# Kernel tuning notes

Hardware: AMD Instinct MI355X
Metric: run time of the kernel (lower is better)

Reference implementation:

```python
import jax, jax.numpy as jnp
import numpy as np
from jax import lax

IN_CH, OUT_CH, K = 64, 64, 3
FAN_IN = 8           # LogicNets-style fan-in per output channel (over C_in*K taps)
IN_SCALE, IN_BITS = 0.0625, 8
OUT_SCALE, OUT_BITS = 0.125, 8


def make_mask(seed=7):
    # Binary mask [OUT_CH, IN_CH, K] with exactly FAN_IN ones per output channel
    rng = np.random.RandomState(seed)
    m = np.zeros((OUT_CH, IN_CH * K), dtype=np.float32)
    for o in range(OUT_CH):
        idx = rng.choice(IN_CH * K, size=FAN_IN, replace=False)
        m[o, idx] = 1.0
    return jnp.asarray(m.reshape(OUT_CH, IN_CH, K))


def fake_quant(v, scale, bits):
    # symmetric fake quantization with straight-through estimator
    qmin = -(2 ** (bits - 1))
    qmax = 2 ** (bits - 1) - 1
    q = jnp.clip(jnp.round(v / scale), qmin, qmax) * scale
    return v + lax.stop_gradient(q - v)


def setup_inputs() -> dict:
    key = jax.random.key(0)
    k1, k2 = jax.random.split(key)
    x = jax.random.normal(k1, (512, IN_CH, 1024), dtype=jnp.float32)
    weight = jax.random.normal(k2, (OUT_CH, IN_CH, K), dtype=jnp.float32) * 0.1
    mask = make_mask()
    return {"x": x, "weight": weight, "mask": mask}


def reference(x, weight, mask):
    # input quant
    xq = fake_quant(x, IN_SCALE, IN_BITS)
    # masked (sparse) conv1d, padding=1 (same length)
    w = weight * mask
    out = lax.conv_general_dilated(
        xq, w,
        window_strides=(1,),
        padding=[(1, 1)],
        dimension_numbers=("NCH", "OIH", "NCH"),
    )
    # output quant
    return fake_quant(out, OUT_SCALE, OUT_BITS)
```

## Files before the change

### kernel.cpp

```cpp
#include <hip/hip_runtime.h>

namespace {
constexpr int kInCh  = 64;
constexpr int kOutCh = 64;
constexpr int kK     = 3;
constexpr int kFanIn = 8;
constexpr int kH     = 1024;
constexpr int kTile  = 128;
constexpr int kRow   = kTile + 8;
constexpr int kBlk   = 512;
}

struct Tap { int off; float w; };

__device__ __forceinline__ float quant_in(float v) {
    float q = rintf(v * 16.0f);
    q = fmaxf(q, -128.0f);
    q = fminf(q, 127.0f);
    return q * 0.0625f;
}

__device__ __forceinline__ float quant_out(float v) {
    float q = rintf(v * 8.0f);
    q = fmaxf(q, -128.0f);
    q = fminf(q, 127.0f);
    return q * 0.125f;
}

__global__ void prep_taps(const float* __restrict__ weight,
                          const float* __restrict__ mask,
                          Tap* __restrict__ taps) {
    __shared__ unsigned long long bal[3];
    const int o    = blockIdx.x;
    const int j    = threadIdx.x;
    const int k    = j >> 6;
    const int ci   = j & 63;
    const int idx  = (o * kInCh + ci) * kK + k;

    const float m = mask[idx];
    const unsigned long long b = __ballot(m != 0.0f);
    if (ci == 0) bal[k] = b;
    __syncthreads();

    const unsigned long long lower = b & ((1ull << ci) - 1ull);
    int rank = __popcll(lower);
    #pragma unroll
    for (int w = 0; w < kK; ++w) if (w < k) rank += __popcll(bal[w]);

    if (m != 0.0f && rank < kFanIn) {
        taps[o * kFanIn + rank].off = (ci * kRow + k + 3) * 4;
        taps[o * kFanIn + rank].w   = weight[idx] * m;
    }
    int total = __popcll(bal[0]) + __popcll(bal[1]) + __popcll(bal[2]);
    if (j >= total && j < kFanIn) {
        taps[o * kFanIn + j].off = 3 * 4;
        taps[o * kFanIn + j].w   = 0.0f;
    }
}

__global__ __launch_bounds__(kBlk, 8) void sparse_conv(
        const float* __restrict__ x,
        const Tap*   __restrict__ taps,
        float*       __restrict__ out) {
    __shared__ float sm[kInCh * kRow];

    const int t    = threadIdx.x;
    const int lane = t & 63;
    const int g    = __builtin_amdgcn_readfirstlane(t >> 6);
    const int h0   = blockIdx.x * kTile;
    const int n    = blockIdx.y;
    const float* __restrict__ xn = x + (size_t)n * kInCh * kH;

    const Tap  myTap = taps[g * 64 + lane];
    const int   vOff = myTap.off;
    const int   vW   = __float_as_int(myTap.w);

    #pragma unroll
    for (int it = 0; it < 4; ++it) {
        int f  = it * kBlk + t;
        int ci = f >> 5;
        int c4 = f & 31;
        float4 v = reinterpret_cast<const float4*>(xn + ci * kH + h0)[c4];
        v.x = quant_in(v.x); v.y = quant_in(v.y);
        v.z = quant_in(v.z); v.w = quant_in(v.w);
        reinterpret_cast<float4*>(&sm[ci * kRow + 4])[c4] = v;
    }
    if (t < 64) {
        int ci = t;
        float4 v = make_float4(0.f, 0.f, 0.f, 0.f);
        if (h0 > 0) v = *reinterpret_cast<const float4*>(xn + ci * kH + h0 - 4);
        v.x = quant_in(v.x); v.y = quant_in(v.y);
        v.z = quant_in(v.z); v.w = quant_in(v.w);
        *reinterpret_cast<float4*>(&sm[ci * kRow]) = v;
    } else if (t < 128) {
        int ci = t - 64;
        float4 v = make_float4(0.f, 0.f, 0.f, 0.f);
        if (h0 + kTile < kH) v = *reinterpret_cast<const float4*>(xn + ci * kH + h0 + kTile);
        v.x = quant_in(v.x); v.y = quant_in(v.y);
        v.z = quant_in(v.z); v.w = quant_in(v.w);
        *reinterpret_cast<float4*>(&sm[ci * kRow + 4 + kTile]) = v;
    }
    __syncthreads();

    const int i  = t & 63;
    const int i4 = i << 2;
    float* __restrict__ outn = out + (size_t)n * kOutCh * kH + h0;
    const char* smb = reinterpret_cast<const char*>(sm);

    #pragma unroll 2
    for (int oo = 0; oo < 8; ++oo) {
        int o = g * 8 + oo;

        float acc0 = 0.f, acc1 = 0.f;
        #pragma unroll
        for (int j = 0; j < kFanIn; ++j) {
            const int l   = oo * 8 + j;
            const int off = __builtin_amdgcn_readlane(vOff, l);
            const float w = __int_as_float(__builtin_amdgcn_readlane(vW, l));
            const float a0 = *reinterpret_cast<const float*>(smb + off + i4);
            const float a1 = *reinterpret_cast<const float*>(smb + off + i4 + 256);
            acc0 = fmaf(w, a0, acc0);
            acc1 = fmaf(w, a1, acc1);
        }
        outn[o * kH + i]      = quant_out(acc0);
        outn[o * kH + i + 64] = quant_out(acc1);
    }
}

extern "C" void kernel_launch(void* const* d_in, const int* in_sizes, int n_in,
                              void* d_out, int out_size, void* d_ws, size_t ws_size,
                              hipStream_t stream) {
    const float* x      = (const float*)d_in[0];
    const float* weight = (const float*)d_in[1];
    const float* mask   = (const float*)d_in[2];
    float* out = (float*)d_out;
    Tap* taps = (Tap*)d_ws;

    const int nBatch = in_sizes[0] / (kInCh * kH);

    prep_taps<<<kOutCh, kInCh * kK, 0, stream>>>(weight, mask, taps);
    dim3 grid(kH / kTile, nBatch);
    sparse_conv<<<grid, kBlk, 0, stream>>>(x, taps, out);
}
```

Baseline: 238.2 us.

## Fuse tap prep into persistent conv kernel with register-prefetched next tile

Removes the separate prep_taps launch by having each block build the sparse tap table in shared memory with ballots. The conv kernel becomes persistent (up to 1024 blocks striding over tiles) and prefetches the next tile's input into registers while computing the current one. The input-quant scale is folded into the weights. This adds per-block table construction and register pressure under the 8-blocks launch bound, and relies on the mask having at most 8 nonzeros per row, with no zero padding of unused tap slots.

Result: slower. 249.7 us (+4.8%).

```diff
diff --git a/kernel.cpp b/kernel.cpp
--- a/kernel.cpp
+++ b/kernel.cpp
@@ -9,15 +9,16 @@
 constexpr int kTile  = 128;
 constexpr int kRow   = kTile + 8;
 constexpr int kBlk   = 512;
+constexpr int kHB    = kH / kTile;
+constexpr int kGrid  = 1024;
 }
 
 struct Tap { int off; float w; };
 
-__device__ __forceinline__ float quant_in(float v) {
+__device__ __forceinline__ float quant_in_i(float v) {
     float q = rintf(v * 16.0f);
     q = fmaxf(q, -128.0f);
-    q = fminf(q, 127.0f);
-    return q * 0.0625f;
+    return fminf(q, 127.0f);
 }
 
 __device__ __forceinline__ float quant_out(float v) {
@@ -27,104 +28,137 @@
     return q * 0.125f;
 }
 
-__global__ void prep_taps(const float* __restrict__ weight,
-                          const float* __restrict__ mask,
-                          Tap* __restrict__ taps) {
-    __shared__ unsigned long long bal[3];
-    const int o    = blockIdx.x;
-    const int j    = threadIdx.x;
-    const int k    = j >> 6;
-    const int ci   = j & 63;
-    const int idx  = (o * kInCh + ci) * kK + k;
-
-    const float m = mask[idx];
-    const unsigned long long b = __ballot(m != 0.0f);
-    if (ci == 0) bal[k] = b;
-    __syncthreads();
-
-    const unsigned long long lower = b & ((1ull << ci) - 1ull);
-    int rank = __popcll(lower);
-    #pragma unroll
-    for (int w = 0; w < kK; ++w) if (w < k) rank += __popcll(bal[w]);
-
-    if (m != 0.0f && rank < kFanIn) {
-        taps[o * kFanIn + rank].off = (ci * kRow + k + 3) * 4;
-        taps[o * kFanIn + rank].w   = weight[idx] * m;
-    }
-    int total = __popcll(bal[0]) + __popcll(bal[1]) + __popcll(bal[2]);
-    if (j >= total && j < kFanIn) {
-        taps[o * kFanIn + j].off = 3 * 4;
-        taps[o * kFanIn + j].w   = 0.0f;
-    }
-}
-
 __global__ __launch_bounds__(kBlk, 8) void sparse_conv(
         const float* __restrict__ x,
-        const Tap*   __restrict__ taps,
-        float*       __restrict__ out) {
+        const float* __restrict__ weight,
+        const float* __restrict__ mask,
+        float*       __restrict__ out,
+        int nTiles) {
     __shared__ float sm[kInCh * kRow];
+    __shared__ Tap   tbl[kBlk];
 
     const int t    = threadIdx.x;
     const int lane = t & 63;
-    const int g    = __builtin_amdgcn_readfirstlane(t >> 6);
-    const int h0   = blockIdx.x * kTile;
-    const int n    = blockIdx.y;
-    const float* __restrict__ xn = x + (size_t)n * kInCh * kH;
+    const int g    = t >> 6;
 
-    const Tap  myTap = taps[g * 64 + lane];
-    const int   vOff = myTap.off;
-    const int   vW   = __float_as_int(myTap.w);
-
-    #pragma unroll
-    for (int it = 0; it < 4; ++it) {
-        int f  = it * kBlk + t;
-        int ci = f >> 5;
-        int c4 = f & 31;
-        float4 v = reinterpret_cast<const float4*>(xn + ci * kH + h0)[c4];
-        v.x = quant_in(v.x); v.y = quant_in(v.y);
-        v.z = quant_in(v.z); v.w = quant_in(v.w);
-        reinterpret_cast<float4*>(&sm[ci * kRow + 4])[c4] = v;
-    }
-    if (t < 64) {
-        int ci = t;
-        float4 v = make_float4(0.f, 0.f, 0.f, 0.f);
-        if (h0 > 0) v = *reinterpret_cast<const float4*>(xn + ci * kH + h0 - 4);
-        v.x = quant_in(v.x); v.y = quant_in(v.y);
-        v.z = quant_in(v.z); v.w = quant_in(v.w);
-        *reinterpret_cast<float4*>(&sm[ci * kRow]) = v;
-    } else if (t < 128) {
-        int ci = t - 64;
-        float4 v = make_float4(0.f, 0.f, 0.f, 0.f);
-        if (h0 + kTile < kH) v = *reinterpret_cast<const float4*>(xn + ci * kH + h0 + kTile);
-        v.x = quant_in(v.x); v.y = quant_in(v.y);
-        v.z = quant_in(v.z); v.w = quant_in(v.w);
-        *reinterpret_cast<float4*>(&sm[ci * kRow + 4 + kTile]) = v;
+    {
+        const unsigned long long low = (1ull << lane) - 1ull;
+        #pragma unroll
+        for (int oo = 0; oo < 8; ++oo) {
+            const int o    = g * 8 + oo;
+            const int base = (o * kInCh + lane) * kK;
+            const float m0 = mask[base + 0], m1 = mask[base + 1], m2 = mask[base + 2];
+            const float w0 = weight[base + 0], w1 = weight[base + 1], w2 = weight[base + 2];
+            const unsigned long long b0 = __ballot(m0 != 0.0f);
+            const unsigned long long b1 = __ballot(m1 != 0.0f);
+            const unsigned long long b2 = __ballot(m2 != 0.0f);
+            const int n0 = __popcll(b0), n1 = __popcll(b1);
+            if (m0 != 0.0f) { int r = __popcll(b0 & low);
+                tbl[o * kFanIn + r].off = (lane * kRow + 3) * 4;
+                tbl[o * kFanIn + r].w   = w0 * m0 * 0.0625f; }
+            if (m1 != 0.0f) { int r = n0 + __popcll(b1 & low);
+                tbl[o * kFanIn + r].off = (lane * kRow + 4) * 4;
+                tbl[o * kFanIn + r].w   = w1 * m1 * 0.0625f; }
+            if (m2 != 0.0f) { int r = n0 + n1 + __popcll(b2 & low);
+                tbl[o * kFanIn + r].off = (lane * kRow + 5) * 4;
+                tbl[o * kFanIn + r].w   = w2 * m2 * 0.0625f; }
+        }
     }
     __syncthreads();
+    const int vOff = tbl[t].off;
+    const int vW   = __float_as_int(tbl[t].w);
 
-    const int i  = t & 63;
-    const int i4 = i << 2;
-    float* __restrict__ outn = out + (size_t)n * kOutCh * kH + h0;
+    const int tci = t >> 5;
+    const int c4  = t & 31;
+    const int i4  = lane << 2;
+
+    float4 r0, r1, r2, r3, rh;
+    const float4 z4 = make_float4(0.f, 0.f, 0.f, 0.f);
+
+#define ISSUE_LOADS(TAU)                                                          \
+    {                                                                             \
+        const int   n_  = (TAU) >> 3;                                             \
+        const int   h0_ = ((TAU) & (kHB - 1)) * kTile;                            \
+        const float* p_ = x + ((size_t)n_ * kInCh) * kH + h0_;                    \
+        r0 = reinterpret_cast<const float4*>(p_ + (tci     ) * kH)[c4];           \
+        r1 = reinterpret_cast<const float4*>(p_ + (tci + 16) * kH)[c4];           \
+        r2 = reinterpret_cast<const float4*>(p_ + (tci + 32) * kH)[c4];           \
+        r3 = reinterpret_cast<const float4*>(p_ + (tci + 48) * kH)[c4];           \
+        if (t < 64) {                                                             \
+            rh = (h0_ > 0) ? *reinterpret_cast<const float4*>(p_ + t * kH - 4)    \
+                           : z4;                                                  \
+        } else if (t < 128) {                                                     \
+            rh = (h0_ + kTile < kH)                                               \
+                 ? *reinterpret_cast<const float4*>(p_ + (t - 64) * kH + kTile)   \
+                 : z4;                                                            \
+        }                                                                         \
+    }
+
+#define STAGE()                                                                   \
+    {                                                                             \
+        float4 q_;                                                                \
+        q_.x = quant_in_i(r0.x); q_.y = quant_in_i(r0.y);                         \
+        q_.z = quant_in_i(r0.z); q_.w = quant_in_i(r0.w);                         \
+        reinterpret_cast<float4*>(&sm[(tci     ) * kRow + 4])[c4] = q_;           \
+        q_.x = quant_in_i(r1.x); q_.y = quant_in_i(r1.y);                         \
+        q_.z = quant_in_i(r1.z); q_.w = quant_in_i(r1.w);                         \
+        reinterpret_cast<float4*>(&sm[(tci + 16) * kRow + 4])[c4] = q_;           \
+        q_.x = quant_in_i(r2.x); q_.y = quant_in_i(r2.y);                         \
+        q_.z = quant_in_i(r2.z); q_.w = quant_in_i(r2.w);                         \
+        reinterpret_cast<float4*>(&sm[(tci + 32) * kRow + 4])[c4] = q_;           \
+        q_.x = quant_in_i(r3.x); q_.y = quant_in_i(r3.y);                         \
+        q_.z = quant_in_i(r3.z); q_.w = quant_in_i(r3.w);                         \
+        reinterpret_cast<float4*>(&sm[(tci + 48) * kRow + 4])[c4] = q_;           \
+        if (t < 64) {                                                             \
+            float4 h_;                                                            \
+            h_.x = quant_in_i(rh.x); h_.y = quant_in_i(rh.y);                     \
+            h_.z = quant_in_i(rh.z); h_.w = quant_in_i(rh.w);                     \
+            *reinterpret_cast<float4*>(&sm[t * kRow]) = h_;                       \
+        } else if (t < 128) {                                                     \
+            float4 h_;                                                            \
+            h_.x = quant_in_i(rh.x); h_.y = quant_in_i(rh.y);                     \
+            h_.z = quant_in_i(rh.z); h_.w = quant_in_i(rh.w);                     \
+            *reinterpret_cast<float4*>(&sm[(t - 64) * kRow + 4 + kTile]) = h_;    \
+        }                                                                         \
+    }
+
+    int tau = blockIdx.x;
+    const int stride = gridDim.x;
     const char* smb = reinterpret_cast<const char*>(sm);
 
-    #pragma unroll 2
-    for (int oo = 0; oo < 8; ++oo) {
-        int o = g * 8 + oo;
+    ISSUE_LOADS(tau);
+    while (tau < nTiles) {
+        STAGE();
+        __syncthreads();
 
-        float acc0 = 0.f, acc1 = 0.f;
-        #pragma unroll
-        for (int j = 0; j < kFanIn; ++j) {
-            const int l   = oo * 8 + j;
-            const int off = __builtin_amdgcn_readlane(vOff, l);
-            const float w = __int_as_float(__builtin_amdgcn_readlane(vW, l));
-            const float a0 = *reinterpret_cast<const float*>(smb + off + i4);
-            const float a1 = *reinterpret_cast<const float*>(smb + off + i4 + 256);
-            acc0 = fmaf(w, a0, acc0);
-            acc1 = fmaf(w, a1, acc1);
+        const int nxt = tau + stride;
+        if (nxt < nTiles) ISSUE_LOADS(nxt);
+
+        float* __restrict__ outn =
+            out + ((size_t)(tau >> 3) * kOutCh) * kH + (tau & (kHB - 1)) * kTile;
+
+        #pragma unroll 2
+        for (int oo = 0; oo < 8; ++oo) {
+            const int o = g * 8 + oo;
+            float acc0 = 0.f, acc1 = 0.f;
+            #pragma unroll
+            for (int j = 0; j < kFanIn; ++j) {
+                const int l   = oo * 8 + j;
+                const int off = __builtin_amdgcn_readlane(vOff, l);
+                const float w = __int_as_float(__builtin_amdgcn_readlane(vW, l));
+                const float a0 = *reinterpret_cast<const float*>(smb + off + i4);
+                const float a1 = *reinterpret_cast<const float*>(smb + off + i4 + 256);
+                acc0 = fmaf(w, a0, acc0);
+                acc1 = fmaf(w, a1, acc1);
+            }
+            outn[o * kH + lane]      = quant_out(acc0);
+            outn[o * kH + lane + 64] = quant_out(acc1);
         }
-        outn[o * kH + i]      = quant_out(acc0);
-        outn[o * kH + i + 64] = quant_out(acc1);
+        __syncthreads();
+        tau = nxt;
     }
+#undef ISSUE_LOADS
+#undef STAGE
 }
 
 extern "C" void kernel_launch(void* const* d_in, const int* in_sizes, int n_in,
@@ -134,11 +168,10 @@
     const float* weight = (const float*)d_in[1];
     const float* mask   = (const float*)d_in[2];
     float* out = (float*)d_out;
-    Tap* taps = (Tap*)d_ws;
 
     const int nBatch = in_sizes[0] / (kInCh * kH);
+    const int nTiles = nBatch * kHB;
+    const int grid   = nTiles < kGrid ? nTiles : kGrid;
 
-    prep_taps<<<kOutCh, kInCh * kK, 0, stream>>>(weight, mask, taps);
-    dim3 grid(kH / kTile, nBatch);
-    sparse_conv<<<grid, kBlk, 0, stream>>>(x, taps, out);
+    sparse_conv<<<grid, kBlk, 0, stream>>>(x, weight, mask, out, nTiles);
 }
```

## Fuse tap preparation into conv kernel and double spatial tile size

Applied to the files above, without the earlier changes.

Removes the separate prep_taps launch: each block builds the sparse tap table in shared memory from weight and mask using wave ballots, and folds the input dequant scale into the weights. The tile grows to 256 positions, so each thread computes four outputs per channel, and all input loads are issued into registers before the table build to overlap latency. The grid is flattened to 1D. In exchange every block rereads the mask and weights, uses more registers and shared memory, and occupancy is lower with launch bounds reduced to 4.

Result: slower. 257.9 us (+8.3%).

```diff
diff --git a/kernel.cpp b/kernel.cpp
--- a/kernel.cpp
+++ b/kernel.cpp
@@ -6,18 +6,18 @@
 constexpr int kK     = 3;
 constexpr int kFanIn = 8;
 constexpr int kH     = 1024;
-constexpr int kTile  = 128;
+constexpr int kTile  = 256;
 constexpr int kRow   = kTile + 8;
 constexpr int kBlk   = 512;
+constexpr int kHB    = kH / kTile;
 }
 
 struct Tap { int off; float w; };
 
-__device__ __forceinline__ float quant_in(float v) {
+__device__ __forceinline__ float quant_in_i(float v) {
     float q = rintf(v * 16.0f);
     q = fmaxf(q, -128.0f);
-    q = fminf(q, 127.0f);
-    return q * 0.0625f;
+    return fminf(q, 127.0f);
 }
 
 __device__ __forceinline__ float quant_out(float v) {
@@ -27,103 +27,102 @@
     return q * 0.125f;
 }
 
-__global__ void prep_taps(const float* __restrict__ weight,
-                          const float* __restrict__ mask,
-                          Tap* __restrict__ taps) {
-    __shared__ unsigned long long bal[3];
-    const int o    = blockIdx.x;
-    const int j    = threadIdx.x;
-    const int k    = j >> 6;
-    const int ci   = j & 63;
-    const int idx  = (o * kInCh + ci) * kK + k;
-
-    const float m = mask[idx];
-    const unsigned long long b = __ballot(m != 0.0f);
-    if (ci == 0) bal[k] = b;
-    __syncthreads();
-
-    const unsigned long long lower = b & ((1ull << ci) - 1ull);
-    int rank = __popcll(lower);
-    #pragma unroll
-    for (int w = 0; w < kK; ++w) if (w < k) rank += __popcll(bal[w]);
-
-    if (m != 0.0f && rank < kFanIn) {
-        taps[o * kFanIn + rank].off = (ci * kRow + k + 3) * 4;
-        taps[o * kFanIn + rank].w   = weight[idx] * m;
-    }
-    int total = __popcll(bal[0]) + __popcll(bal[1]) + __popcll(bal[2]);
-    if (j >= total && j < kFanIn) {
-        taps[o * kFanIn + j].off = 3 * 4;
-        taps[o * kFanIn + j].w   = 0.0f;
-    }
-}
-
-__global__ __launch_bounds__(kBlk, 8) void sparse_conv(
+__global__ __launch_bounds__(kBlk, 4) void sparse_conv(
         const float* __restrict__ x,
-        const Tap*   __restrict__ taps,
+        const float* __restrict__ weight,
+        const float* __restrict__ mask,
         float*       __restrict__ out) {
     __shared__ float sm[kInCh * kRow];
+    __shared__ Tap   tbl[kBlk];
 
     const int t    = threadIdx.x;
     const int lane = t & 63;
     const int g    = __builtin_amdgcn_readfirstlane(t >> 6);
-    const int h0   = blockIdx.x * kTile;
-    const int n    = blockIdx.y;
-    const float* __restrict__ xn = x + (size_t)n * kInCh * kH;
+    const int tau  = blockIdx.x;
+    const int n    = tau >> 2;
+    const int h0   = (tau & (kHB - 1)) * kTile;
+    const float* __restrict__ xn = x + (size_t)n * kInCh * kH + h0;
 
-    const Tap  myTap = taps[g * 64 + lane];
-    const int   vOff = myTap.off;
-    const int   vW   = __float_as_int(myTap.w);
+    float4 r[8];
+    #pragma unroll
+    for (int it = 0; it < 8; ++it)
+        r[it] = reinterpret_cast<const float4*>(xn + (it * 8 + g) * kH)[lane];
+    float4 rh = make_float4(0.f, 0.f, 0.f, 0.f);
+    if (t < 64) {
+        if (h0 > 0) rh = *reinterpret_cast<const float4*>(xn + t * kH - 4);
+    } else if (t < 128) {
+        if (h0 + kTile < kH) rh = *reinterpret_cast<const float4*>(xn + (t - 64) * kH + kTile);
+    }
+
+    {
+        const unsigned long long low = (1ull << lane) - 1ull;
+        #pragma unroll
+        for (int oo = 0; oo < 8; ++oo) {
+            const int o    = g * 8 + oo;
+            const int base = (o * kInCh + lane) * kK;
+            const float m0 = mask[base + 0], m1 = mask[base + 1], m2 = mask[base + 2];
+            const float w0 = weight[base + 0], w1 = weight[base + 1], w2 = weight[base + 2];
+            const unsigned long long b0 = __ballot(m0 != 0.0f);
+            const unsigned long long b1 = __ballot(m1 != 0.0f);
+            const unsigned long long b2 = __ballot(m2 != 0.0f);
+            const int n0 = __popcll(b0), n1 = __popcll(b1);
+            if (m0 != 0.0f) { int rk = __popcll(b0 & low);
+                tbl[o * kFanIn + rk].off = (lane * kRow + 3) * 4;
+                tbl[o * kFanIn + rk].w   = w0 * m0 * 0.0625f; }
+            if (m1 != 0.0f) { int rk = n0 + __popcll(b1 & low);
+                tbl[o * kFanIn + rk].off = (lane * kRow + 4) * 4;
+                tbl[o * kFanIn + rk].w   = w1 * m1 * 0.0625f; }
+            if (m2 != 0.0f) { int rk = n0 + n1 + __popcll(b2 & low);
+                tbl[o * kFanIn + rk].off = (lane * kRow + 5) * 4;
+                tbl[o * kFanIn + rk].w   = w2 * m2 * 0.0625f; }
+        }
+    }
+    const int vOff = tbl[t].off;
+    const int vW   = __float_as_int(tbl[t].w);
 
     #pragma unroll
-    for (int it = 0; it < 4; ++it) {
-        int f  = it * kBlk + t;
-        int ci = f >> 5;
-        int c4 = f & 31;
-        float4 v = reinterpret_cast<const float4*>(xn + ci * kH + h0)[c4];
-        v.x = quant_in(v.x); v.y = quant_in(v.y);
-        v.z = quant_in(v.z); v.w = quant_in(v.w);
-        reinterpret_cast<float4*>(&sm[ci * kRow + 4])[c4] = v;
+    for (int it = 0; it < 8; ++it) {
+        float4 q;
+        q.x = quant_in_i(r[it].x); q.y = quant_in_i(r[it].y);
+        q.z = quant_in_i(r[it].z); q.w = quant_in_i(r[it].w);
+        reinterpret_cast<float4*>(&sm[(it * 8 + g) * kRow + 4])[lane] = q;
     }
     if (t < 64) {
-        int ci = t;
-        float4 v = make_float4(0.f, 0.f, 0.f, 0.f);
-        if (h0 > 0) v = *reinterpret_cast<const float4*>(xn + ci * kH + h0 - 4);
-        v.x = quant_in(v.x); v.y = quant_in(v.y);
-        v.z = quant_in(v.z); v.w = quant_in(v.w);
-        *reinterpret_cast<float4*>(&sm[ci * kRow]) = v;
+        float4 q;
+        q.x = quant_in_i(rh.x); q.y = quant_in_i(rh.y);
+        q.z = quant_in_i(rh.z); q.w = quant_in_i(rh.w);
+        *reinterpret_cast<float4*>(&sm[t * kRow]) = q;
     } else if (t < 128) {
-        int ci = t - 64;
-        float4 v = make_float4(0.f, 0.f, 0.f, 0.f);
-        if (h0 + kTile < kH) v = *reinterpret_cast<const float4*>(xn + ci * kH + h0 + kTile);
-        v.x = quant_in(v.x); v.y = quant_in(v.y);
-        v.z = quant_in(v.z); v.w = quant_in(v.w);
-        *reinterpret_cast<float4*>(&sm[ci * kRow + 4 + kTile]) = v;
+        float4 q;
+        q.x = quant_in_i(rh.x); q.y = quant_in_i(rh.y);
+        q.z = quant_in_i(rh.z); q.w = quant_in_i(rh.w);
+        *reinterpret_cast<float4*>(&sm[(t - 64) * kRow + 4 + kTile]) = q;
     }
     __syncthreads();
 
-    const int i  = t & 63;
-    const int i4 = i << 2;
+    const int i4 = lane << 2;
+    const char* smb = reinterpret_cast<const char*>(sm);
     float* __restrict__ outn = out + (size_t)n * kOutCh * kH + h0;
-    const char* smb = reinterpret_cast<const char*>(sm);
 
     #pragma unroll 2
     for (int oo = 0; oo < 8; ++oo) {
-        int o = g * 8 + oo;
-
-        float acc0 = 0.f, acc1 = 0.f;
+        const int o = g * 8 + oo;
+        float a0 = 0.f, a1 = 0.f, a2 = 0.f, a3 = 0.f;
         #pragma unroll
         for (int j = 0; j < kFanIn; ++j) {
             const int l   = oo * 8 + j;
             const int off = __builtin_amdgcn_readlane(vOff, l);
             const float w = __int_as_float(__builtin_amdgcn_readlane(vW, l));
-            const float a0 = *reinterpret_cast<const float*>(smb + off + i4);
-            const float a1 = *reinterpret_cast<const float*>(smb + off + i4 + 256);
-            acc0 = fmaf(w, a0, acc0);
-            acc1 = fmaf(w, a1, acc1);
+            const char* p = smb + off + i4;
+            a0 = fmaf(w, *reinterpret_cast<const float*>(p      ), a0);
+            a1 = fmaf(w, *reinterpret_cast<const float*>(p + 256), a1);
+            a2 = fmaf(w, *reinterpret_cast<const float*>(p + 512), a2);
+            a3 = fmaf(w, *reinterpret_cast<const float*>(p + 768), a3);
         }
-        outn[o * kH + i]      = quant_out(acc0);
-        outn[o * kH + i + 64] = quant_out(acc1);
+        outn[o * kH + lane]       = quant_out(a0);
+        outn[o * kH + lane +  64] = quant_out(a1);
+        outn[o * kH + lane + 128] = quant_out(a2);
+        outn[o * kH + lane + 192] = quant_out(a3);
     }
 }
 
@@ -134,11 +133,9 @@
     const float* weight = (const float*)d_in[1];
     const float* mask   = (const float*)d_in[2];
     float* out = (float*)d_out;
-    Tap* taps = (Tap*)d_ws;
 
     const int nBatch = in_sizes[0] / (kInCh * kH);
+    const int grid   = nBatch * kHB;
 
-    prep_taps<<<kOutCh, kInCh * kK, 0, stream>>>(weight, mask, taps);
-    dim3 grid(kH / kTile, nBatch);
-    sparse_conv<<<grid, kBlk, 0, stream>>>(x, taps, out);
+    sparse_conv<<<grid, kBlk, 0, stream>>>(x, weight, mask, out);
 }
```

## Halve tile and block size, batch global loads, fold input scale into weights

Applied to the files above, without the earlier changes.

Cuts the spatial tile to 64 and the block to 256 threads, so each wave handles 16 output channels with one accumulator per lane. All global loads are issued into registers before quantization and the LDS stores, so more loads are in flight. Halo loads shrink to single scalars. Taps are now read straight from global memory with uniform addresses instead of readlane broadcasts, and the input scale 1/16 is folded into the weights so the LDS holds integer-valued floats. This doubles the number of blocks and the halo overhead per tile, and tap loads now go through the scalar cache.

After: 238.1 us. Within noise of the previous version (-0.0%).

```diff
diff --git a/kernel.cpp b/kernel.cpp
--- a/kernel.cpp
+++ b/kernel.cpp
@@ -6,18 +6,18 @@
 constexpr int kK     = 3;
 constexpr int kFanIn = 8;
 constexpr int kH     = 1024;
-constexpr int kTile  = 128;
+constexpr int kTile  = 64;
 constexpr int kRow   = kTile + 8;
-constexpr int kBlk   = 512;
+constexpr int kBlk   = 256;
+constexpr int kHB    = kH / kTile;
 }
 
 struct Tap { int off; float w; };
 
-__device__ __forceinline__ float quant_in(float v) {
+__device__ __forceinline__ float quant_in_i(float v) {
     float q = rintf(v * 16.0f);
     q = fmaxf(q, -128.0f);
-    q = fminf(q, 127.0f);
-    return q * 0.0625f;
+    return fminf(q, 127.0f);
 }
 
 __device__ __forceinline__ float quant_out(float v) {
@@ -48,12 +48,12 @@
     for (int w = 0; w < kK; ++w) if (w < k) rank += __popcll(bal[w]);
 
     if (m != 0.0f && rank < kFanIn) {
-        taps[o * kFanIn + rank].off = (ci * kRow + k + 3) * 4;
-        taps[o * kFanIn + rank].w   = weight[idx] * m;
+        taps[o * kFanIn + rank].off = ci * kRow + k + 3;
+        taps[o * kFanIn + rank].w   = weight[idx] * m * 0.0625f;
     }
     int total = __popcll(bal[0]) + __popcll(bal[1]) + __popcll(bal[2]);
     if (j >= total && j < kFanIn) {
-        taps[o * kFanIn + j].off = 3 * 4;
+        taps[o * kFanIn + j].off = 3;
         taps[o * kFanIn + j].w   = 0.0f;
     }
 }
@@ -69,61 +69,52 @@
     const int g    = __builtin_amdgcn_readfirstlane(t >> 6);
     const int h0   = blockIdx.x * kTile;
     const int n    = blockIdx.y;
-    const float* __restrict__ xn = x + (size_t)n * kInCh * kH;
+    const float* __restrict__ xn = x + (size_t)n * kInCh * kH + h0;
 
-    const Tap  myTap = taps[g * 64 + lane];
-    const int   vOff = myTap.off;
-    const int   vW   = __float_as_int(myTap.w);
+    float4 r[4];
+    #pragma unroll
+    for (int it = 0; it < 4; ++it) {
+        const int f  = it * kBlk + t;
+        const int ci = f >> 4;
+        const int c4 = f & 15;
+        r[it] = reinterpret_cast<const float4*>(xn + ci * kH)[c4];
+    }
+    float hv = 0.f;
+    if (t < 64) {
+        if (h0 > 0) hv = xn[t * kH - 1];
+    } else if (t < 128) {
+        if (h0 + kTile < kH) hv = xn[(t - 64) * kH + kTile];
+    }
 
     #pragma unroll
     for (int it = 0; it < 4; ++it) {
-        int f  = it * kBlk + t;
-        int ci = f >> 5;
-        int c4 = f & 31;
-        float4 v = reinterpret_cast<const float4*>(xn + ci * kH + h0)[c4];
-        v.x = quant_in(v.x); v.y = quant_in(v.y);
-        v.z = quant_in(v.z); v.w = quant_in(v.w);
-        reinterpret_cast<float4*>(&sm[ci * kRow + 4])[c4] = v;
+        const int f  = it * kBlk + t;
+        const int ci = f >> 4;
+        const int c4 = f & 15;
+        float4 q;
+        q.x = quant_in_i(r[it].x); q.y = quant_in_i(r[it].y);
+        q.z = quant_in_i(r[it].z); q.w = quant_in_i(r[it].w);
+        reinterpret_cast<float4*>(&sm[ci * kRow + 4])[c4] = q;
     }
     if (t < 64) {
-        int ci = t;
-        float4 v = make_float4(0.f, 0.f, 0.f, 0.f);
-        if (h0 > 0) v = *reinterpret_cast<const float4*>(xn + ci * kH + h0 - 4);
-        v.x = quant_in(v.x); v.y = quant_in(v.y);
-        v.z = quant_in(v.z); v.w = quant_in(v.w);
-        *reinterpret_cast<float4*>(&sm[ci * kRow]) = v;
+        sm[t * kRow + 3] = quant_in_i(hv);
     } else if (t < 128) {
-        int ci = t - 64;
-        float4 v = make_float4(0.f, 0.f, 0.f, 0.f);
-        if (h0 + kTile < kH) v = *reinterpret_cast<const float4*>(xn + ci * kH + h0 + kTile);
-        v.x = quant_in(v.x); v.y = quant_in(v.y);
-        v.z = quant_in(v.z); v.w = quant_in(v.w);
-        *reinterpret_cast<float4*>(&sm[ci * kRow + 4 + kTile]) = v;
+        sm[(t - 64) * kRow + 4 + kTile] = quant_in_i(hv);
     }
     __syncthreads();
 
-    const int i  = t & 63;
-    const int i4 = i << 2;
     float* __restrict__ outn = out + (size_t)n * kOutCh * kH + h0;
-    const char* smb = reinterpret_cast<const char*>(sm);
 
-    #pragma unroll 2
-    for (int oo = 0; oo < 8; ++oo) {
-        int o = g * 8 + oo;
-
-        float acc0 = 0.f, acc1 = 0.f;
+    #pragma unroll 4
+    for (int oo = 0; oo < 16; ++oo) {
+        const int o = g * 16 + oo;
+        const Tap* __restrict__ tp = taps + o * kFanIn;
+        float acc = 0.f;
         #pragma unroll
         for (int j = 0; j < kFanIn; ++j) {
-            const int l   = oo * 8 + j;
-            const int off = __builtin_amdgcn_readlane(vOff, l);
-            const float w = __int_as_float(__builtin_amdgcn_readlane(vW, l));
-            const float a0 = *reinterpret_cast<const float*>(smb + off + i4);
-            const float a1 = *reinterpret_cast<const float*>(smb + off + i4 + 256);
-            acc0 = fmaf(w, a0, acc0);
-            acc1 = fmaf(w, a1, acc1);
+            acc = fmaf(tp[j].w, sm[tp[j].off + lane], acc);
         }
-        outn[o * kH + i]      = quant_out(acc0);
-        outn[o * kH + i + 64] = quant_out(acc1);
+        outn[o * kH + lane] = quant_out(acc);
     }
 }
 
@@ -139,6 +130,6 @@
     const int nBatch = in_sizes[0] / (kInCh * kH);
 
     prep_taps<<<kOutCh, kInCh * kK, 0, stream>>>(weight, mask, taps);
-    dim3 grid(kH / kTile, nBatch);
+    dim3 grid(kHB, nBatch);
     sparse_conv<<<grid, kBlk, 0, stream>>>(x, taps, out);
 }
```
